# Kernel optimization log

Hardware: AMD Instinct MI355X
Metric: run time of the kernel (lower is better)

Reference implementation:

```python
import jax, jax.numpy as jnp
import numpy as np

B, J, D, H, W, AE, GH, NA, EH, L = 64, 20000, 32, 64, 4, 16, 24, 5000, 128, 32


def _ln(x, g=None, b=None, eps=1e-5):
    mu = x.mean(-1, keepdims=True)
    var = jnp.mean((x - mu) ** 2, axis=-1, keepdims=True)
    y = (x - mu) * jax.lax.rsqrt(var + eps)
    if g is not None:
        y = y * g + b
    return y


def setup_inputs():
    key = jax.random.key(0)
    ks = jax.random.split(key, 12)
    def rn(k, shape, s):
        return (jax.random.normal(k, shape) * s).astype(jnp.float32)
    return {
        "x": jax.random.normal(ks[0], (B, J), jnp.float32),
        "mask": jax.random.randint(ks[1], (B, J), 0, 2, jnp.int32),
        "atse_idx": jax.random.randint(ks[2], (J,), 0, NA, jnp.int32),
        "feature_embedding": jax.random.normal(ks[3], (J, D), jnp.float32),
        "atse_embedding": jax.random.normal(ks[4], (NA, AE), jnp.float32),
        "h_W1": rn(ks[5], (1 + D, H), 0.15), "h_b1": jnp.zeros((H,), jnp.float32),
        "h_ln1_g": jnp.ones((H,), jnp.float32), "h_ln1_b": jnp.zeros((H,), jnp.float32),
        "h_W2": rn(ks[6], (H, D), 0.12), "h_b2": jnp.zeros((D,), jnp.float32),
        "h_ln2_g": jnp.ones((D,), jnp.float32), "h_ln2_b": jnp.zeros((D,), jnp.float32),
        "g_W1": rn(ks[7], (D + AE, GH), 0.14), "g_b1": jnp.zeros((GH,), jnp.float32),
        "g_W2": rn(ks[8], (GH, W), 0.2), "g_b2": jnp.zeros((W,), jnp.float32),
        "c_W": rn(ks[9], (W * D, D), 0.09), "c_b": jnp.zeros((D,), jnp.float32),
        "c_ln_g": jnp.ones((D,), jnp.float32), "c_ln_b": jnp.zeros((D,), jnp.float32),
        "e_W1": rn(ks[10], (D, EH), 0.18), "e_b1": jnp.zeros((EH,), jnp.float32),
        "e_W2": rn(ks[11], (EH, 2 * L), 0.09), "e_b2": jnp.zeros((2 * L,), jnp.float32),
    }


def _forward(x, mask, atse_idx, feature_embedding, atse_embedding,
             h_W1, h_b1, h_ln1_g, h_ln1_b, h_W2, h_b2, h_ln2_g, h_ln2_b,
             g_W1, g_b1, g_W2, g_b2, c_W, c_b, c_ln_g, c_ln_b,
             e_W1, e_b1, e_W2, e_b2):
    TEMP = 1.0  # temperature_fixed=True -> scale = temperature_value
    Bv, Jv = x.shape
    Dv = feature_embedding.shape[1]
    # h-layer on all (b, j) pairs; LayerNorm/ReLU are per-row so this equals the
    # per-sample gather version on observed rows (unobserved rows get zero weight below).
    h_in = jnp.concatenate(
        [x[..., None], jnp.broadcast_to(feature_embedding[None], (Bv, Jv, Dv))], axis=-1)
    h = jax.nn.relu(_ln(h_in @ h_W1 + h_b1, h_ln1_g, h_ln1_b))
    h_out = jax.nn.relu(_ln(h @ h_W2 + h_b2, h_ln2_g, h_ln2_b))  # [B, J, D]
    # gate: [h_out | E_atse(j)] -> W head logits
    ae = atse_embedding[atse_idx]  # [J, AE]
    gate_in = jnp.concatenate(
        [h_out, jnp.broadcast_to(ae[None], (Bv, Jv, ae.shape[1]))], axis=-1)
    raw = jax.nn.relu(gate_in @ g_W1 + g_b1) @ g_W2 + g_b2  # [B, J, W]
    logits = jnp.clip(raw * TEMP, -10.0, 10.0)
    obs = mask.astype(bool)
    masked = jnp.where(obs[..., None], logits, -1e9)
    weights = jax.nn.softmax(masked, axis=1)  # softmax over observed junctions per head
    head_sums = jnp.einsum('bjw,bjd->bwd', weights, h_out)  # [B, W, D]
    Wn, Dn = head_sums.shape[1], head_sums.shape[2]
    combined = jax.nn.relu(_ln(head_sums.reshape(Bv, Wn * Dn) @ c_W + c_b, c_ln_g, c_ln_b))
    combined = jnp.where(obs.any(axis=1)[:, None], combined, 0.0)  # empty-mask rows -> zeros
    # encoder_mlp: scvi FCLayers, 2 layers, LayerNorm (no affine) + ReLU each
    e1 = jax.nn.relu(_ln(combined @ e_W1 + e_b1))
    mu_logvar = jax.nn.relu(_ln(e1 @ e_W2 + e_b2))
    mu, logvar = jnp.split(mu_logvar, 2, axis=-1)
    return mu, logvar


def reference(x, mask, atse_idx, feature_embedding, atse_embedding,
              h_W1, h_b1, h_ln1_g, h_ln1_b, h_W2, h_b2, h_ln2_g, h_ln2_b,
              g_W1, g_b1, g_W2, g_b2, c_W, c_b, c_ln_g, c_ln_b,
              e_W1, e_b1, e_W2, e_b2):
    return _forward(x, mask, atse_idx, feature_embedding, atse_embedding,
                    h_W1, h_b1, h_ln1_g, h_ln1_b, h_W2, h_b2, h_ln2_g, h_ln2_b,
                    g_W1, g_b1, g_W2, g_b2, c_W, c_b, c_ln_g, c_ln_b,
                    e_W1, e_b1, e_W2, e_b2)
```

## Files before the change

kernel.cpp:

```cpp
#include <hip/hip_runtime.h>
#include <hip/hip_bf16.h>
#include <math.h>

#define Bv 64
#define Jv 20000
#define NBT 8
#define NYB 125
#define ITERS 5

typedef __attribute__((ext_vector_type(8))) short short8;
typedef __attribute__((ext_vector_type(4))) float f32x4;
typedef __attribute__((ext_vector_type(2))) float f32x2;
typedef __attribute__((ext_vector_type(2))) unsigned int u32x2;

union U8 { short8 s; unsigned int u[4]; };

__device__ __forceinline__ unsigned short f2bf(float f) {
  unsigned int u = __float_as_uint(f);
  u += 0x7FFFu + ((u >> 16) & 1u);
  return (unsigned short)(u >> 16);
}
__device__ __forceinline__ unsigned int pkbf(float a, float b) {
  __hip_bfloat162 h = __float22bfloat162_rn(make_float2(a, b));
  union { __hip_bfloat162 h; unsigned int u; } c;
  c.h = h;
  return c.u;
}

__device__ __forceinline__ f32x2 pk_fma(f32x2 a, f32x2 b, f32x2 c) {
  return __builtin_elementwise_fma(a, b, c);
}
__device__ __forceinline__ f32x2 pk_max0(f32x2 a) {
  f32x2 z = {0.f, 0.f};
  return __builtin_elementwise_max(a, z);
}

template <int CTRL>
__device__ __forceinline__ float dppadd(float v) {
  int t = __builtin_amdgcn_update_dpp(0, __float_as_int(v), CTRL, 0xF, 0xF, true);
  return v + __int_as_float(t);
}
__device__ __forceinline__ float pl16sum(float v) {
  float a = v, b;
  asm("v_mov_b32 %1, %0\n\t"
      "v_permlane16_swap_b32 %0, %1"
      : "+v"(a), "=&v"(b));
  return a + b;
}
__device__ __forceinline__ float pl32sum(float v) {
  float a = v, b;
  asm("v_mov_b32 %1, %0\n\t"
      "v_permlane32_swap_b32 %0, %1"
      : "+v"(a), "=&v"(b));
  return a + b;
}

__global__ __launch_bounds__(256) void pe_fused(
    const float* __restrict__ x, const int* __restrict__ mask,
    const int* __restrict__ atse_idx, const float* __restrict__ fe,
    const float* __restrict__ ae,
    const float* __restrict__ hW1, const float* __restrict__ hb1,
    const float* __restrict__ hl1g, const float* __restrict__ hl1b,
    const float* __restrict__ hW2, const float* __restrict__ hb2,
    const float* __restrict__ hl2g, const float* __restrict__ hl2b,
    const float* __restrict__ gW1, const float* __restrict__ gb1,
    const float* __restrict__ gW2, const float* __restrict__ gb2,
    float* __restrict__ acc_g, float* __restrict__ se_g) {
  __shared__ __align__(16) float s_pg[32 * 68];
  __shared__ __align__(16) float s_gb[32 * 24 + 16];
  __shared__ __align__(16) float s_pair[256 * 4];
  __shared__ __align__(16) float s_w0[64], s_w0g[64], s_l1g[64], s_l1b[64];
  __shared__ __align__(16) float s_b2[32], s_l2g[32], s_l2b[32];
  __shared__ __align__(16) float s_gb1[24], s_gW2[96];
  __shared__ float s_gb2[4], s_scal[2];
  __shared__ __align__(16) float s_gW1aT[24 * 16];
  __shared__ unsigned char s_mk[256];
  __shared__ __align__(16) unsigned short s_gW1bf[32 * 24];
  __shared__ __align__(16) unsigned short s_ovl[256 * 36];

  int tid = threadIdx.x;
  int btile = blockIdx.x;
  int ytile = blockIdx.y;
  int lane = tid & 63, wv = tid >> 6;
  int li = lane & 15, quad = lane >> 4;
  unsigned short* s_h = s_ovl;

#define AEROW(j) ((float*)((char*)s_ovl + ((j) >> 3) * 4608 + 3968) + ((j) & 7) * 20)

  for (int i = tid; i < 768; i += 256) s_gW1bf[i] = f2bf(gW1[i]);
  for (int i = tid; i < 384; i += 256)
    s_gW1aT[i] = gW1[768 + (i & 15) * 24 + (i >> 4)];
  if (tid < 96) s_gW2[tid] = gW2[tid];
  if (tid < 64) { s_w0[tid] = hW1[tid]; s_l1g[tid] = hl1g[tid]; s_l1b[tid] = hl1b[tid]; }
  if (tid < 32) { s_b2[tid] = hb2[tid]; s_l2g[tid] = hl2g[tid]; s_l2b[tid] = hl2b[tid]; }
  if (tid < 24) s_gb1[tid] = gb1[tid];
  if (tid < 4) s_gb2[tid] = gb2[tid];
  if (tid >= 224 && tid < 240) s_gb[32 * 24 + (tid - 224)] = 0.f;

  short8 bW2[2][2];
#pragma unroll
  for (int kt = 0; kt < 2; ++kt)
#pragma unroll
    for (int nt = 0; nt < 2; ++nt) {
      U8 t;
#pragma unroll
      for (int p = 0; p < 4; ++p) {
        float lo = hW2[(kt * 32 + quad * 8 + 2 * p) * 32 + nt * 16 + li];
        float hi = hW2[(kt * 32 + quad * 8 + 2 * p + 1) * 32 + nt * 16 + li];
        t.u[p] = pkbf(lo, hi);
      }
      bW2[kt][nt] = t.s;
    }
  U8 bH;
#pragma unroll
  for (int p = 0; p < 4; ++p) {
    float lo = hW1[(1 + quad * 8 + 2 * p) * 64 + wv * 16 + li];
    float hi = hW1[(1 + quad * 8 + 2 * p + 1) * 64 + wv * 16 + li];
    bH.u[p] = pkbf(lo, hi);
  }
  float hb = hb1[wv * 16 + li];

  __syncthreads();
  if (tid < 64) s_w0g[tid] = s_w0[tid] * s_l1g[tid];
  if (tid == 64) {
    float sw = 0.f, qw = 0.f;
    for (int k = 0; k < 64; ++k) { float w = s_w0[k]; sw += w; qw = fmaf(w, w, qw); }
    s_scal[0] = sw; s_scal[1] = qw;
  }
  short8 aG0, aG1;
#pragma unroll
  for (int i = 0; i < 8; ++i) {
    int k = quad * 8 + i;
    aG0[i] = (short)s_gW1bf[k * 24 + li];
    aG1[i] = (li < 8) ? (short)s_gW1bf[k * 24 + 16 + li] : (short)0;
  }

  f32x4 racc[2][2];
#pragma unroll
  for (int a = 0; a < 2; ++a)
#pragma unroll
    for (int c = 0; c < 2; ++c) {
      racc[a][c][0] = 0.f; racc[a][c][1] = 0.f; racc[a][c][2] = 0.f; racc[a][c][3] = 0.f;
    }
  float seacc[2] = {0.f, 0.f};

  int jp8 = tid >> 3, b8 = tid & 7;

  for (int it = 0; it < ITERS; ++it) {
    int J0 = (ytile * ITERS + it) * 32;

    if (tid < 32) {
      int ai = atse_idx[J0 + tid];
      const float4* av4 = (const float4*)(ae + (size_t)ai * 16);
      float* ar = AEROW(tid);
#pragma unroll
      for (int q = 0; q < 4; ++q) *(float4*)(ar + q * 4) = av4[q];
    }
    size_t xoff = (size_t)(btile * 8 + b8) * Jv + J0 + jp8;
    float xv = x[xoff];
    int mk = mask[xoff];
    {
      f32x4 cP;
#pragma unroll
      for (int mt = 0; mt < 2; ++mt) {
        cP[0] = hb; cP[1] = hb; cP[2] = hb; cP[3] = hb;
        const float* fp = fe + (size_t)(J0 + mt * 16 + li) * 32 + quad * 8;
        float4 f0 = *(const float4*)fp;
        float4 f1 = *(const float4*)(fp + 4);
        U8 aF;
        aF.u[0] = pkbf(f0.x, f0.y); aF.u[1] = pkbf(f0.z, f0.w);
        aF.u[2] = pkbf(f1.x, f1.y); aF.u[3] = pkbf(f1.z, f1.w);
        cP = __builtin_amdgcn_mfma_f32_16x16x32_bf16(aF.s, bH.s, cP, 0, 0, 0);
#pragma unroll
        for (int r = 0; r < 4; ++r)
          s_pg[(mt * 16 + quad * 4 + r) * 68 + wv * 16 + li] = cP[r];
      }
    }
    __syncthreads();

    {
      int c0 = b8 * 3;
      const f32x2* ar2 = (const f32x2*)AEROW(jp8);
      f32x2 A[8];
#pragma unroll
      for (int a = 0; a < 8; ++a) A[a] = ar2[a];
#pragma unroll
      for (int c = 0; c < 3; ++c) {
        const f32x2* tr2 = (const f32x2*)(s_gW1aT + (c0 + c) * 16);
        f32x2 g2 = {s_gb1[c0 + c], 0.f};
#pragma unroll
        for (int a = 0; a < 8; ++a) g2 = pk_fma(A[a], tr2[a], g2);
        s_gb[jp8 * 24 + c0 + c] = g2.x + g2.y;
      }
    }
    {
      const f32x2* pp2 = (const f32x2*)(s_pg + jp8 * 68 + b8 * 8);
      const f32x2* ww2 = (const f32x2*)(s_w0 + b8 * 8);
      f32x2 p2[4] = {pp2[0], pp2[1], pp2[2], pp2[3]};
      f32x2 s2 = (p2[0] + p2[1]) + (p2[2] + p2[3]);
      f32x2 q2 = pk_fma(p2[0], p2[0],
                 pk_fma(p2[1], p2[1],
                 pk_fma(p2[2], p2[2], p2[3] * p2[3])));
      f32x2 d2 = pk_fma(p2[0], ww2[0],
                 pk_fma(p2[1], ww2[1],
                 pk_fma(p2[2], ww2[2], p2[3] * ww2[3])));
      float sp = s2.x + s2.y, qp = q2.x + q2.y, dwp = d2.x + d2.y;
      sp = dppadd<0xB1>(sp); sp = dppadd<0x4E>(sp); sp = dppadd<0x141>(sp);
      qp = dppadd<0xB1>(qp); qp = dppadd<0x4E>(qp); qp = dppadd<0x141>(qp);
      dwp = dppadd<0xB1>(dwp); dwp = dppadd<0x4E>(dwp); dwp = dppadd<0x141>(dwp);
      if (b8 == 0) *(float4*)(s_pg + jp8 * 68 + 64) = make_float4(sp, qp, dwp, 0.f);
    }
    {
      float4 exv = *(const float4*)(s_pg + jp8 * 68 + 64);
      float mu1 = fmaf(xv, s_scal[0], exv.x) * 0.015625f;
      float Et2 = fmaf(xv * xv, s_scal[1], fmaf(2.0f * xv, exv.z, exv.y)) * 0.015625f;
      float rs1 = rsqrtf(fmaxf(Et2 - mu1 * mu1, 0.f) + 1e-5f);
      *(float4*)(s_pair + tid * 4) = make_float4(xv * rs1, rs1, -mu1 * rs1, 0.f);
      s_mk[tid] = (unsigned char)mk;
    }

    {
      f32x4 cd[4][2];
      float b2a = s_b2[li], b2b = s_b2[16 + li];
#pragma unroll
      for (int t = 0; t < 4; ++t) {
        cd[t][0][0] = b2a; cd[t][0][1] = b2a; cd[t][0][2] = b2a; cd[t][0][3] = b2a;
        cd[t][1][0] = b2b; cd[t][1][1] = b2b; cd[t][1][2] = b2b; cd[t][1][3] = b2b;
      }
#pragma unroll
      for (int kt = 0; kt < 2; ++kt) {
        int base = kt * 32 + quad * 8;
        float4 wg0 = *(const float4*)(s_w0g + base);
        float4 wg1 = *(const float4*)(s_w0g + base + 4);
        float4 gg0 = *(const float4*)(s_l1g + base);
        float4 gg1 = *(const float4*)(s_l1g + base + 4);
        float4 bb0 = *(const float4*)(s_l1b + base);
        float4 bb1 = *(const float4*)(s_l1b + base + 4);
        f32x2 wg2[4] = {{wg0.x, wg0.y}, {wg0.z, wg0.w}, {wg1.x, wg1.y}, {wg1.z, wg1.w}};
        f32x2 gg2[4] = {{gg0.x, gg0.y}, {gg0.z, gg0.w}, {gg1.x, gg1.y}, {gg1.z, gg1.w}};
        f32x2 bb2[4] = {{bb0.x, bb0.y}, {bb0.z, bb0.w}, {bb1.x, bb1.y}, {bb1.z, bb1.w}};
#pragma unroll
        for (int t = 0; t < 4; ++t) {
          int mrow = wv * 64 + t * 16 + li;
          float4 pr = *(const float4*)(s_pair + mrow * 4);
          f32x2 prx = {pr.x, pr.x}, pry = {pr.y, pr.y}, prz = {pr.z, pr.z};
          const float* pgp = s_pg + (mrow >> 3) * 68 + base;
          float4 p0 = *(const float4*)pgp;
          float4 p1 = *(const float4*)(pgp + 4);
          f32x2 pv2[4] = {{p0.x, p0.y}, {p0.z, p0.w}, {p1.x, p1.y}, {p1.z, p1.w}};
          U8 a8;
#pragma unroll
          for (int i = 0; i < 4; ++i) {
            f32x2 av2 = pk_max0(pk_fma(pk_fma(pry, pv2[i], prz), gg2[i],
                                       pk_fma(prx, wg2[i], bb2[i])));
            a8.u[i] = pkbf(av2.x, av2.y);
          }
          cd[t][0] = __builtin_amdgcn_mfma_f32_16x16x32_bf16(a8.s, bW2[kt][0], cd[t][0], 0, 0, 0);
          cd[t][1] = __builtin_amdgcn_mfma_f32_16x16x32_bf16(a8.s, bW2[kt][1], cd[t][1], 0, 0, 0);
        }
      }
      float g0 = s_l2g[li], be0 = s_l2b[li];
      float g1v = s_l2g[16 + li], be1 = s_l2b[16 + li];
#pragma unroll
      for (int t = 0; t < 4; ++t) {
        float sum[4], sq[4];
#pragma unroll
        for (int r = 0; r < 4; ++r) {
          float a = cd[t][0][r], b = cd[t][1][r];
          sum[r] = a + b;
          sq[r] = fmaf(a, a, b * b);
        }
#pragma unroll
        for (int r = 0; r < 4; ++r) {
          sum[r] = dppadd<0xB1>(sum[r]); sum[r] = dppadd<0x4E>(sum[r]);
          sum[r] = dppadd<0x124>(sum[r]); sum[r] = dppadd<0x128>(sum[r]);
          sq[r] = dppadd<0xB1>(sq[r]); sq[r] = dppadd<0x4E>(sq[r]);
          sq[r] = dppadd<0x124>(sq[r]); sq[r] = dppadd<0x128>(sq[r]);
        }
#pragma unroll
        for (int r = 0; r < 4; ++r) {
          float mu = sum[r] * 0.03125f;
          float var = sq[r] * 0.03125f - mu * mu;
          float rs2 = rsqrtf(fmaxf(var, 0.f) + 1e-5f);
          int m = wv * 64 + t * 16 + quad * 4 + r;
          float h0 = fmaxf(fmaf((cd[t][0][r] - mu) * rs2, g0, be0), 0.f);
          float h1 = fmaxf(fmaf((cd[t][1][r] - mu) * rs2, g1v, be1), 0.f);
          s_h[m * 36 + li] = f2bf(h0);
          s_h[m * 36 + 16 + li] = f2bf(h1);
        }
      }
    }

    {
      float4 gw4[2][4];
#pragma unroll
      for (int mt = 0; mt < 2; ++mt)
#pragma unroll
        for (int r = 0; r < 4; ++r) {
          int c = mt * 16 + quad * 4 + r;
          gw4[mt][r] = (c < 24) ? ((const float4*)s_gW2)[c]
                                : make_float4(0.f, 0.f, 0.f, 0.f);
        }
#pragma unroll
      for (int nt = 0; nt < 4; ++nt) {
        int m = wv * 64 + nt * 16 + li;
        U8 bu;
        const u32x2* hp2 = (const u32x2*)(s_h + m * 36 + quad * 8);
        u32x2 h01 = hp2[0], h23 = hp2[1];
        bu.u[0] = h01[0]; bu.u[1] = h01[1]; bu.u[2] = h23[0]; bu.u[3] = h23[1];
        int j = m >> 3;
        f32x4 c0, c1;
#pragma unroll
        for (int r = 0; r < 4; ++r) {
          c0[r] = s_gb[j * 24 + quad * 4 + r];
          c1[r] = s_gb[j * 24 + 16 + quad * 4 + r];
        }
        c0 = __builtin_amdgcn_mfma_f32_16x16x32_bf16(aG0, bu.s, c0, 0, 0, 0);
        c1 = __builtin_amdgcn_mfma_f32_16x16x32_bf16(aG1, bu.s, c1, 0, 0, 0);
        f32x2 r01 = {s_gb2[0], s_gb2[1]};
        f32x2 r23 = {s_gb2[2], s_gb2[3]};
#pragma unroll
        for (int r = 0; r < 4; ++r) {
          float v0 = fmaxf(c0[r], 0.f);
          float v1 = fmaxf(c1[r], 0.f);
          f32x2 v0b = {v0, v0}, v1b = {v1, v1};
          float4 ga = gw4[0][r], gb = gw4[1][r];
          f32x2 ga01 = {ga.x, ga.y}, ga23 = {ga.z, ga.w};
          f32x2 gb01 = {gb.x, gb.y}, gb23 = {gb.z, gb.w};
          r01 = pk_fma(v0b, ga01, pk_fma(v1b, gb01, r01));
          r23 = pk_fma(v0b, ga23, pk_fma(v1b, gb23, r23));
        }
        float r0 = pl32sum(pl16sum(r01.x));
        float r1 = pl32sum(pl16sum(r01.y));
        float r2 = pl32sum(pl16sum(r23.x));
        float r3 = pl32sum(pl16sum(r23.y));
        r0 = fminf(fmaxf(r0, -10.f), 10.f);
        r1 = fminf(fmaxf(r1, -10.f), 10.f);
        r2 = fminf(fmaxf(r2, -10.f), 10.f);
        r3 = fminf(fmaxf(r3, -10.f), 10.f);
        bool act = (s_mk[m] != 0);
        float e0 = act ? __expf(r0 - 10.f) : 0.f;
        float e1 = act ? __expf(r1 - 10.f) : 0.f;
        float e2 = act ? __expf(r2 - 10.f) : 0.f;
        float e3 = act ? __expf(r3 - 10.f) : 0.f;
        if (quad == 0) *(float4*)(s_pair + m * 4) = make_float4(e0, e1, e2, e3);
      }
    }
    __syncthreads();

    {
      const float* s_e2 = s_pair;
#pragma unroll
      for (int bs = 0; bs < 2; ++bs) {
        int b = wv * 2 + bs;
        float ev[8];
        float sep = 0.f;
#pragma unroll
        for (int i = 0; i < 8; ++i) {
          float v = s_e2[((quad * 8 + i) * 8 + b) * 4 + (li & 3)];
          v = (li < 4) ? v : 0.f;
          ev[i] = v;
          sep += v;
        }
        seacc[bs] += sep;
        U8 a8;
        a8.u[0] = pkbf(ev[0], ev[1]); a8.u[1] = pkbf(ev[2], ev[3]);
        a8.u[2] = pkbf(ev[4], ev[5]); a8.u[3] = pkbf(ev[6], ev[7]);
#pragma unroll
        for (int half = 0; half < 2; ++half) {
          U8 bh;
#pragma unroll
          for (int p = 0; p < 4; ++p) {
            unsigned int lo = s_h[((quad * 8 + 2 * p) * 8 + b) * 36 + half * 16 + li];
            unsigned int hi = s_h[((quad * 8 + 2 * p + 1) * 8 + b) * 36 + half * 16 + li];
            bh.u[p] = lo | (hi << 16);
          }
          racc[bs][half] = __builtin_amdgcn_mfma_f32_16x16x32_bf16(a8.s, bh.s, racc[bs][half], 0, 0, 0);
        }
      }
    }
    __syncthreads();
  }

#pragma unroll
  for (int bs = 0; bs < 2; ++bs) {
    float se = seacc[bs];
    se = pl32sum(pl16sum(se));
    if (quad == 0) {
      int bg = btile * 8 + wv * 2 + bs;
      float* dst = acc_g + (size_t)bg * 128;
#pragma unroll
      for (int half = 0; half < 2; ++half)
#pragma unroll
        for (int r = 0; r < 4; ++r)
          atomicAdd(dst + r * 32 + half * 16 + li, racc[bs][half][r]);
      if (li < 4) atomicAdd(&se_g[bg * 4 + li], se);
    }
  }
#undef AEROW
}

__global__ __launch_bounds__(64) void pe_tail(
    const float* __restrict__ acc_g, const float* __restrict__ se_g,
    const float* __restrict__ cW, const float* __restrict__ cb,
    const float* __restrict__ clng, const float* __restrict__ clnb,
    const float* __restrict__ eW1, const float* __restrict__ eb1,
    const float* __restrict__ eW2, const float* __restrict__ eb2,
    float* __restrict__ out) {
  int b = blockIdx.x;
  int lane = threadIdx.x;
  __shared__ float s_hs[128], s_comb[32], s_e1[128];

  float se0 = se_g[b * 4 + 0];
  bool empty = !(se0 > 0.0f);
  float inv[4];
#pragma unroll
  for (int w = 0; w < 4; ++w) {
    float sw = se_g[b * 4 + w];
    inv[w] = empty ? 0.0f : 1.0f / sw;
  }
  s_hs[lane] = acc_g[b * 128 + lane] * inv[lane >> 5];
  s_hs[lane + 64] = acc_g[b * 128 + lane + 64] * inv[(lane + 64) >> 5];
  __syncthreads();

  if (lane < 32) {
    float cp = cb[lane];
#pragma unroll 8
    for (int i = 0; i < 128; ++i) cp = fmaf(s_hs[i], cW[i * 32 + lane], cp);
    float ssum = cp;
#pragma unroll
    for (int off = 16; off > 0; off >>= 1) ssum += __shfl_xor(ssum, off, 32);
    float mu = ssum * (1.0f / 32.0f);
    float dd = cp - mu;
    float sq = dd * dd;
#pragma unroll
    for (int off = 16; off > 0; off >>= 1) sq += __shfl_xor(sq, off, 32);
    float rs = rsqrtf(sq * (1.0f / 32.0f) + 1e-5f);
    float comb = fmaxf(fmaf(dd * rs, clng[lane], clnb[lane]), 0.0f);
    if (empty) comb = 0.0f;
    s_comb[lane] = comb;
  }
  __syncthreads();

  float v0 = eb1[lane], v1 = eb1[lane + 64];
#pragma unroll
  for (int i = 0; i < 32; ++i) {
    float c = s_comb[i];
    v0 = fmaf(c, eW1[i * 128 + lane], v0);
    v1 = fmaf(c, eW1[i * 128 + lane + 64], v1);
  }
  float ssum = v0 + v1;
#pragma unroll
  for (int off = 32; off > 0; off >>= 1) ssum += __shfl_xor(ssum, off, 64);
  float mu = ssum * (1.0f / 128.0f);
  float d0 = v0 - mu, d1 = v1 - mu;
  float sq = fmaf(d0, d0, d1 * d1);
#pragma unroll
  for (int off = 32; off > 0; off >>= 1) sq += __shfl_xor(sq, off, 64);
  float rs = rsqrtf(sq * (1.0f / 128.0f) + 1e-5f);
  s_e1[lane] = fmaxf(d0 * rs, 0.0f);
  s_e1[lane + 64] = fmaxf(d1 * rs, 0.0f);
  __syncthreads();

  float v = eb2[lane];
#pragma unroll 8
  for (int i = 0; i < 128; ++i) v = fmaf(s_e1[i], eW2[i * 64 + lane], v);
  ssum = v;
#pragma unroll
  for (int off = 32; off > 0; off >>= 1) ssum += __shfl_xor(ssum, off, 64);
  mu = ssum * (1.0f / 64.0f);
  float dv = v - mu;
  sq = dv * dv;
#pragma unroll
  for (int off = 32; off > 0; off >>= 1) sq += __shfl_xor(sq, off, 64);
  rs = rsqrtf(sq * (1.0f / 64.0f) + 1e-5f);
  float o = fmaxf(dv * rs, 0.0f);
  if (lane < 32)
    out[b * 32 + lane] = o;
  else
    out[Bv * 32 + b * 32 + (lane - 32)] = o;
}

extern "C" void kernel_launch(void* const* d_in, const int* in_sizes, int n_in,
                              void* d_out, int out_size, void* d_ws, size_t ws_size,
                              hipStream_t stream) {
  const float* x    = (const float*)d_in[0];
  const int* mask   = (const int*)d_in[1];
  const int* atse   = (const int*)d_in[2];
  const float* fe   = (const float*)d_in[3];
  const float* ae   = (const float*)d_in[4];
  const float* hW1  = (const float*)d_in[5];
  const float* hb1  = (const float*)d_in[6];
  const float* hl1g = (const float*)d_in[7];
  const float* hl1b = (const float*)d_in[8];
  const float* hW2  = (const float*)d_in[9];
  const float* hb2  = (const float*)d_in[10];
  const float* hl2g = (const float*)d_in[11];
  const float* hl2b = (const float*)d_in[12];
  const float* gW1  = (const float*)d_in[13];
  const float* gb1  = (const float*)d_in[14];
  const float* gW2  = (const float*)d_in[15];
  const float* gb2  = (const float*)d_in[16];
  const float* cW   = (const float*)d_in[17];
  const float* cb   = (const float*)d_in[18];
  const float* clng = (const float*)d_in[19];
  const float* clnb = (const float*)d_in[20];
  const float* eW1  = (const float*)d_in[21];
  const float* eb1  = (const float*)d_in[22];
  const float* eW2  = (const float*)d_in[23];
  const float* eb2  = (const float*)d_in[24];
  float* out = (float*)d_out;

  float* ws = (float*)d_ws;
  float* accg = ws;
  float* seg  = accg + Bv * 128;

  hipMemsetAsync(accg, 0, (Bv * 128 + Bv * 4) * sizeof(float), stream);

  pe_fused<<<dim3(NBT, NYB), dim3(256), 0, stream>>>(
      x, mask, atse, fe, ae, hW1, hb1, hl1g, hl1b, hW2, hb2, hl2g, hl2b,
      gW1, gb1, gW2, gb2, accg, seg);
  pe_tail<<<dim3(Bv), dim3(64), 0, stream>>>(
      accg, seg, cW, cb, clng, clnb, eW1, eb1, eW2, eb2, out);
}
```

Before: 212.0 us.

## Drop per-block junction loop; launch one block per 32-junction tile

Removes the 5-iteration loop over junction tiles inside each block and launches five times as many blocks along the junction axis, with each block handling a single 32-junction tile. Per-tile results are atomically added straight to the global accumulators instead of being held in registers across iterations. The change also loads the gate bias with float4 reads. The aim is more parallelism and fewer block-internal barriers, at the cost of five times the global atomics and repeating the per-block weight setup in every block.

```diff
diff --git a/kernel.cpp b/kernel.cpp
--- a/kernel.cpp
+++ b/kernel.cpp
@@ -5,8 +5,7 @@
 #define Bv 64
 #define Jv 20000
 #define NBT 8
-#define NYB 125
-#define ITERS 5
+#define NYB 625
 
 typedef __attribute__((ext_vector_type(8))) short short8;
 typedef __attribute__((ext_vector_type(4))) float f32x4;
@@ -87,6 +86,8 @@
 
 #define AEROW(j) ((float*)((char*)s_ovl + ((j) >> 3) * 4608 + 3968) + ((j) & 7) * 20)
 
+  int J0 = ytile * 32;
+
   for (int i = tid; i < 768; i += 256) s_gW1bf[i] = f2bf(gW1[i]);
   for (int i = tid; i < 384; i += 256)
     s_gW1aT[i] = gW1[768 + (i & 15) * 24 + (i >> 4)];
@@ -135,266 +136,244 @@
     aG1[i] = (li < 8) ? (short)s_gW1bf[k * 24 + 16 + li] : (short)0;
   }
 
-  f32x4 racc[2][2];
-#pragma unroll
-  for (int a = 0; a < 2; ++a)
-#pragma unroll
-    for (int c = 0; c < 2; ++c) {
-      racc[a][c][0] = 0.f; racc[a][c][1] = 0.f; racc[a][c][2] = 0.f; racc[a][c][3] = 0.f;
-    }
-  float seacc[2] = {0.f, 0.f};
-
   int jp8 = tid >> 3, b8 = tid & 7;
 
-  for (int it = 0; it < ITERS; ++it) {
-    int J0 = (ytile * ITERS + it) * 32;
-
-    if (tid < 32) {
-      int ai = atse_idx[J0 + tid];
-      const float4* av4 = (const float4*)(ae + (size_t)ai * 16);
-      float* ar = AEROW(tid);
-#pragma unroll
-      for (int q = 0; q < 4; ++q) *(float4*)(ar + q * 4) = av4[q];
-    }
-    size_t xoff = (size_t)(btile * 8 + b8) * Jv + J0 + jp8;
-    float xv = x[xoff];
-    int mk = mask[xoff];
-    {
-      f32x4 cP;
-#pragma unroll
-      for (int mt = 0; mt < 2; ++mt) {
-        cP[0] = hb; cP[1] = hb; cP[2] = hb; cP[3] = hb;
-        const float* fp = fe + (size_t)(J0 + mt * 16 + li) * 32 + quad * 8;
-        float4 f0 = *(const float4*)fp;
-        float4 f1 = *(const float4*)(fp + 4);
-        U8 aF;
-        aF.u[0] = pkbf(f0.x, f0.y); aF.u[1] = pkbf(f0.z, f0.w);
-        aF.u[2] = pkbf(f1.x, f1.y); aF.u[3] = pkbf(f1.z, f1.w);
-        cP = __builtin_amdgcn_mfma_f32_16x16x32_bf16(aF.s, bH.s, cP, 0, 0, 0);
-#pragma unroll
-        for (int r = 0; r < 4; ++r)
-          s_pg[(mt * 16 + quad * 4 + r) * 68 + wv * 16 + li] = cP[r];
-      }
-    }
-    __syncthreads();
-
-    {
-      int c0 = b8 * 3;
-      const f32x2* ar2 = (const f32x2*)AEROW(jp8);
-      f32x2 A[8];
-#pragma unroll
-      for (int a = 0; a < 8; ++a) A[a] = ar2[a];
-#pragma unroll
-      for (int c = 0; c < 3; ++c) {
-        const f32x2* tr2 = (const f32x2*)(s_gW1aT + (c0 + c) * 16);
-        f32x2 g2 = {s_gb1[c0 + c], 0.f};
-#pragma unroll
-        for (int a = 0; a < 8; ++a) g2 = pk_fma(A[a], tr2[a], g2);
-        s_gb[jp8 * 24 + c0 + c] = g2.x + g2.y;
-      }
-    }
-    {
-      const f32x2* pp2 = (const f32x2*)(s_pg + jp8 * 68 + b8 * 8);
-      const f32x2* ww2 = (const f32x2*)(s_w0 + b8 * 8);
-      f32x2 p2[4] = {pp2[0], pp2[1], pp2[2], pp2[3]};
-      f32x2 s2 = (p2[0] + p2[1]) + (p2[2] + p2[3]);
-      f32x2 q2 = pk_fma(p2[0], p2[0],
-                 pk_fma(p2[1], p2[1],
-                 pk_fma(p2[2], p2[2], p2[3] * p2[3])));
-      f32x2 d2 = pk_fma(p2[0], ww2[0],
-                 pk_fma(p2[1], ww2[1],
-                 pk_fma(p2[2], ww2[2], p2[3] * ww2[3])));
-      float sp = s2.x + s2.y, qp = q2.x + q2.y, dwp = d2.x + d2.y;
-      sp = dppadd<0xB1>(sp); sp = dppadd<0x4E>(sp); sp = dppadd<0x141>(sp);
-      qp = dppadd<0xB1>(qp); qp = dppadd<0x4E>(qp); qp = dppadd<0x141>(qp);
-      dwp = dppadd<0xB1>(dwp); dwp = dppadd<0x4E>(dwp); dwp = dppadd<0x141>(dwp);
-      if (b8 == 0) *(float4*)(s_pg + jp8 * 68 + 64) = make_float4(sp, qp, dwp, 0.f);
-    }
-    {
-      float4 exv = *(const float4*)(s_pg + jp8 * 68 + 64);
-      float mu1 = fmaf(xv, s_scal[0], exv.x) * 0.015625f;
-      float Et2 = fmaf(xv * xv, s_scal[1], fmaf(2.0f * xv, exv.z, exv.y)) * 0.015625f;
-      float rs1 = rsqrtf(fmaxf(Et2 - mu1 * mu1, 0.f) + 1e-5f);
-      *(float4*)(s_pair + tid * 4) = make_float4(xv * rs1, rs1, -mu1 * rs1, 0.f);
-      s_mk[tid] = (unsigned char)mk;
-    }
-
-    {
-      f32x4 cd[4][2];
-      float b2a = s_b2[li], b2b = s_b2[16 + li];
+  if (tid < 32) {
+    int ai = atse_idx[J0 + tid];
+    const float4* av4 = (const float4*)(ae + (size_t)ai * 16);
+    float* ar = AEROW(tid);
+#pragma unroll
+    for (int q = 0; q < 4; ++q) *(float4*)(ar + q * 4) = av4[q];
+  }
+  size_t xoff = (size_t)(btile * 8 + b8) * Jv + J0 + jp8;
+  float xv = x[xoff];
+  int mk = mask[xoff];
+  {
+    f32x4 cP;
+#pragma unroll
+    for (int mt = 0; mt < 2; ++mt) {
+      cP[0] = hb; cP[1] = hb; cP[2] = hb; cP[3] = hb;
+      const float* fp = fe + (size_t)(J0 + mt * 16 + li) * 32 + quad * 8;
+      float4 f0 = *(const float4*)fp;
+      float4 f1 = *(const float4*)(fp + 4);
+      U8 aF;
+      aF.u[0] = pkbf(f0.x, f0.y); aF.u[1] = pkbf(f0.z, f0.w);
+      aF.u[2] = pkbf(f1.x, f1.y); aF.u[3] = pkbf(f1.z, f1.w);
+      cP = __builtin_amdgcn_mfma_f32_16x16x32_bf16(aF.s, bH.s, cP, 0, 0, 0);
+#pragma unroll
+      for (int r = 0; r < 4; ++r)
+        s_pg[(mt * 16 + quad * 4 + r) * 68 + wv * 16 + li] = cP[r];
+    }
+  }
+  __syncthreads();
+
+  {
+    int c0 = b8 * 3;
+    const f32x2* ar2 = (const f32x2*)AEROW(jp8);
+    f32x2 A[8];
+#pragma unroll
+    for (int a = 0; a < 8; ++a) A[a] = ar2[a];
+#pragma unroll
+    for (int c = 0; c < 3; ++c) {
+      const f32x2* tr2 = (const f32x2*)(s_gW1aT + (c0 + c) * 16);
+      f32x2 g2 = {s_gb1[c0 + c], 0.f};
+#pragma unroll
+      for (int a = 0; a < 8; ++a) g2 = pk_fma(A[a], tr2[a], g2);
+      s_gb[jp8 * 24 + c0 + c] = g2.x + g2.y;
+    }
+  }
+  {
+    const f32x2* pp2 = (const f32x2*)(s_pg + jp8 * 68 + b8 * 8);
+    const f32x2* ww2 = (const f32x2*)(s_w0 + b8 * 8);
+    f32x2 p2[4] = {pp2[0], pp2[1], pp2[2], pp2[3]};
+    f32x2 s2 = (p2[0] + p2[1]) + (p2[2] + p2[3]);
+    f32x2 q2 = pk_fma(p2[0], p2[0],
+               pk_fma(p2[1], p2[1],
+               pk_fma(p2[2], p2[2], p2[3] * p2[3])));
+    f32x2 d2 = pk_fma(p2[0], ww2[0],
+               pk_fma(p2[1], ww2[1],
+               pk_fma(p2[2], ww2[2], p2[3] * ww2[3])));
+    float sp = s2.x + s2.y, qp = q2.x + q2.y, dwp = d2.x + d2.y;
+    sp = dppadd<0xB1>(sp); sp = dppadd<0x4E>(sp); sp = dppadd<0x141>(sp);
+    qp = dppadd<0xB1>(qp); qp = dppadd<0x4E>(qp); qp = dppadd<0x141>(qp);
+    dwp = dppadd<0xB1>(dwp); dwp = dppadd<0x4E>(dwp); dwp = dppadd<0x141>(dwp);
+    if (b8 == 0) *(float4*)(s_pg + jp8 * 68 + 64) = make_float4(sp, qp, dwp, 0.f);
+  }
+  {
+    float4 exv = *(const float4*)(s_pg + jp8 * 68 + 64);
+    float mu1 = fmaf(xv, s_scal[0], exv.x) * 0.015625f;
+    float Et2 = fmaf(xv * xv, s_scal[1], fmaf(2.0f * xv, exv.z, exv.y)) * 0.015625f;
+    float rs1 = rsqrtf(fmaxf(Et2 - mu1 * mu1, 0.f) + 1e-5f);
+    *(float4*)(s_pair + tid * 4) = make_float4(xv * rs1, rs1, -mu1 * rs1, 0.f);
+    s_mk[tid] = (unsigned char)mk;
+  }
+
+  {
+    f32x4 cd[4][2];
+    float b2a = s_b2[li], b2b = s_b2[16 + li];
+#pragma unroll
+    for (int t = 0; t < 4; ++t) {
+      cd[t][0][0] = b2a; cd[t][0][1] = b2a; cd[t][0][2] = b2a; cd[t][0][3] = b2a;
+      cd[t][1][0] = b2b; cd[t][1][1] = b2b; cd[t][1][2] = b2b; cd[t][1][3] = b2b;
+    }
+#pragma unroll
+    for (int kt = 0; kt < 2; ++kt) {
+      int base = kt * 32 + quad * 8;
+      float4 wg0 = *(const float4*)(s_w0g + base);
+      float4 wg1 = *(const float4*)(s_w0g + base + 4);
+      float4 gg0 = *(const float4*)(s_l1g + base);
+      float4 gg1 = *(const float4*)(s_l1g + base + 4);
+      float4 bb0 = *(const float4*)(s_l1b + base);
+      float4 bb1 = *(const float4*)(s_l1b + base + 4);
+      f32x2 wg2[4] = {{wg0.x, wg0.y}, {wg0.z, wg0.w}, {wg1.x, wg1.y}, {wg1.z, wg1.w}};
+      f32x2 gg2[4] = {{gg0.x, gg0.y}, {gg0.z, gg0.w}, {gg1.x, gg1.y}, {gg1.z, gg1.w}};
+      f32x2 bb2[4] = {{bb0.x, bb0.y}, {bb0.z, bb0.w}, {bb1.x, bb1.y}, {bb1.z, bb1.w}};
 #pragma unroll
       for (int t = 0; t < 4; ++t) {
-        cd[t][0][0] = b2a; cd[t][0][1] = b2a; cd[t][0][2] = b2a; cd[t][0][3] = b2a;
-        cd[t][1][0] = b2b; cd[t][1][1] = b2b; cd[t][1][2] = b2b; cd[t][1][3] = b2b;
-      }
-#pragma unroll
-      for (int kt = 0; kt < 2; ++kt) {
-        int base = kt * 32 + quad * 8;
-        float4 wg0 = *(const float4*)(s_w0g + base);
-        float4 wg1 = *(const float4*)(s_w0g + base + 4);
-        float4 gg0 = *(const float4*)(s_l1g + base);
-        float4 gg1 = *(const float4*)(s_l1g + base + 4);
-        float4 bb0 = *(const float4*)(s_l1b + base);
-        float4 bb1 = *(const float4*)(s_l1b + base + 4);
-        f32x2 wg2[4] = {{wg0.x, wg0.y}, {wg0.z, wg0.w}, {wg1.x, wg1.y}, {wg1.z, wg1.w}};
-        f32x2 gg2[4] = {{gg0.x, gg0.y}, {gg0.z, gg0.w}, {gg1.x, gg1.y}, {gg1.z, gg1.w}};
-        f32x2 bb2[4] = {{bb0.x, bb0.y}, {bb0.z, bb0.w}, {bb1.x, bb1.y}, {bb1.z, bb1.w}};
-#pragma unroll
-        for (int t = 0; t < 4; ++t) {
-          int mrow = wv * 64 + t * 16 + li;
-          float4 pr = *(const float4*)(s_pair + mrow * 4);
-          f32x2 prx = {pr.x, pr.x}, pry = {pr.y, pr.y}, prz = {pr.z, pr.z};
-          const float* pgp = s_pg + (mrow >> 3) * 68 + base;
-          float4 p0 = *(const float4*)pgp;
-          float4 p1 = *(const float4*)(pgp + 4);
-          f32x2 pv2[4] = {{p0.x, p0.y}, {p0.z, p0.w}, {p1.x, p1.y}, {p1.z, p1.w}};
-          U8 a8;
-#pragma unroll
-          for (int i = 0; i < 4; ++i) {
-            f32x2 av2 = pk_max0(pk_fma(pk_fma(pry, pv2[i], prz), gg2[i],
-                                       pk_fma(prx, wg2[i], bb2[i])));
-            a8.u[i] = pkbf(av2.x, av2.y);
-          }
-          cd[t][0] = __builtin_amdgcn_mfma_f32_16x16x32_bf16(a8.s, bW2[kt][0], cd[t][0], 0, 0, 0);
-          cd[t][1] = __builtin_amdgcn_mfma_f32_16x16x32_bf16(a8.s, bW2[kt][1], cd[t][1], 0, 0, 0);
+        int mrow = wv * 64 + t * 16 + li;
+        float4 pr = *(const float4*)(s_pair + mrow * 4);
+        f32x2 prx = {pr.x, pr.x}, pry = {pr.y, pr.y}, prz = {pr.z, pr.z};
+        const float* pgp = s_pg + (mrow >> 3) * 68 + base;
+        float4 p0 = *(const float4*)pgp;
+        float4 p1 = *(const float4*)(pgp + 4);
+        f32x2 pv2[4] = {{p0.x, p0.y}, {p0.z, p0.w}, {p1.x, p1.y}, {p1.z, p1.w}};
+        U8 a8;
+#pragma unroll
+        for (int i = 0; i < 4; ++i) {
+          f32x2 av2 = pk_max0(pk_fma(pk_fma(pry, pv2[i], prz), gg2[i],
+                                     pk_fma(prx, wg2[i], bb2[i])));
+          a8.u[i] = pkbf(av2.x, av2.y);
         }
-      }
-      float g0 = s_l2g[li], be0 = s_l2b[li];
-      float g1v = s_l2g[16 + li], be1 = s_l2b[16 + li];
-#pragma unroll
-      for (int t = 0; t < 4; ++t) {
-        float sum[4], sq[4];
-#pragma unroll
-        for (int r = 0; r < 4; ++r) {
-          float a = cd[t][0][r], b = cd[t][1][r];
-          sum[r] = a + b;
-          sq[r] = fmaf(a, a, b * b);
+        cd[t][0] = __builtin_amdgcn_mfma_f32_16x16x32_bf16(a8.s, bW2[kt][0], cd[t][0], 0, 0, 0);
+        cd[t][1] = __builtin_amdgcn_mfma_f32_16x16x32_bf16(a8.s, bW2[kt][1], cd[t][1], 0, 0, 0);
+      }
+    }
+    float g0 = s_l2g[li], be0 = s_l2b[li];
+    float g1v = s_l2g[16 + li], be1 = s_l2b[16 + li];
+#pragma unroll
+    for (int t = 0; t < 4; ++t) {
+      float sum[4], sq[4];
+#pragma unroll
+      for (int r = 0; r < 4; ++r) {
+        float a = cd[t][0][r], b = cd[t][1][r];
+        sum[r] = a + b;
+        sq[r] = fmaf(a, a, b * b);
+      }
+#pragma unroll
+      for (int r = 0; r < 4; ++r) {
+        sum[r] = dppadd<0xB1>(sum[r]); sum[r] = dppadd<0x4E>(sum[r]);
+        sum[r] = dppadd<0x124>(sum[r]); sum[r] = dppadd<0x128>(sum[r]);
+        sq[r] = dppadd<0xB1>(sq[r]); sq[r] = dppadd<0x4E>(sq[r]);
+        sq[r] = dppadd<0x124>(sq[r]); sq[r] = dppadd<0x128>(sq[r]);
+      }
+#pragma unroll
+      for (int r = 0; r < 4; ++r) {
+        float mu = sum[r] * 0.03125f;
+        float var = sq[r] * 0.03125f - mu * mu;
+        float rs2 = rsqrtf(fmaxf(var, 0.f) + 1e-5f);
+        int m = wv * 64 + t * 16 + quad * 4 + r;
+        float h0 = fmaxf(fmaf((cd[t][0][r] - mu) * rs2, g0, be0), 0.f);
+        float h1 = fmaxf(fmaf((cd[t][1][r] - mu) * rs2, g1v, be1), 0.f);
+        s_h[m * 36 + li] = f2bf(h0);
+        s_h[m * 36 + 16 + li] = f2bf(h1);
+      }
+    }
+  }
+
+  {
+    float4 gw4[2][4];
+#pragma unroll
+    for (int mt = 0; mt < 2; ++mt)
+#pragma unroll
+      for (int r = 0; r < 4; ++r) {
+        int c = mt * 16 + quad * 4 + r;
+        gw4[mt][r] = (c < 24) ? ((const float4*)s_gW2)[c]
+                              : make_float4(0.f, 0.f, 0.f, 0.f);
+      }
+#pragma unroll
+    for (int nt = 0; nt < 4; ++nt) {
+      int m = wv * 64 + nt * 16 + li;
+      U8 bu;
+      const u32x2* hp2 = (const u32x2*)(s_h + m * 36 + quad * 8);
+      u32x2 h01 = hp2[0], h23 = hp2[1];
+      bu.u[0] = h01[0]; bu.u[1] = h01[1]; bu.u[2] = h23[0]; bu.u[3] = h23[1];
+      int j = m >> 3;
+      float4 cc0 = *(const float4*)(s_gb + j * 24 + quad * 4);
+      float4 cc1 = *(const float4*)(s_gb + j * 24 + 16 + quad * 4);
+      f32x4 c0, c1;
+      c0[0] = cc0.x; c0[1] = cc0.y; c0[2] = cc0.z; c0[3] = cc0.w;
+      c1[0] = cc1.x; c1[1] = cc1.y; c1[2] = cc1.z; c1[3] = cc1.w;
+      c0 = __builtin_amdgcn_mfma_f32_16x16x32_bf16(aG0, bu.s, c0, 0, 0, 0);
+      c1 = __builtin_amdgcn_mfma_f32_16x16x32_bf16(aG1, bu.s, c1, 0, 0, 0);
+      f32x2 r01 = {s_gb2[0], s_gb2[1]};
+      f32x2 r23 = {s_gb2[2], s_gb2[3]};
+#pragma unroll
+      for (int r = 0; r < 4; ++r) {
+        float v0 = fmaxf(c0[r], 0.f);
+        float v1 = fmaxf(c1[r], 0.f);
+        f32x2 v0b = {v0, v0}, v1b = {v1, v1};
+        float4 ga = gw4[0][r], gb = gw4[1][r];
+        f32x2 ga01 = {ga.x, ga.y}, ga23 = {ga.z, ga.w};
+        f32x2 gb01 = {gb.x, gb.y}, gb23 = {gb.z, gb.w};
+        r01 = pk_fma(v0b, ga01, pk_fma(v1b, gb01, r01));
+        r23 = pk_fma(v0b, ga23, pk_fma(v1b, gb23, r23));
+      }
+      float r0 = pl32sum(pl16sum(r01.x));
+      float r1 = pl32sum(pl16sum(r01.y));
+      float r2 = pl32sum(pl16sum(r23.x));
+      float r3 = pl32sum(pl16sum(r23.y));
+      r0 = fminf(fmaxf(r0, -10.f), 10.f);
+      r1 = fminf(fmaxf(r1, -10.f), 10.f);
+      r2 = fminf(fmaxf(r2, -10.f), 10.f);
+      r3 = fminf(fmaxf(r3, -10.f), 10.f);
+      bool act = (s_mk[m] != 0);
+      float e0 = act ? __expf(r0 - 10.f) : 0.f;
+      float e1 = act ? __expf(r1 - 10.f) : 0.f;
+      float e2 = act ? __expf(r2 - 10.f) : 0.f;
+      float e3 = act ? __expf(r3 - 10.f) : 0.f;
+      if (quad == 0) *(float4*)(s_pair + m * 4) = make_float4(e0, e1, e2, e3);
+    }
+  }
+  __syncthreads();
+
+  {
+    const float* s_e2 = s_pair;
+#pragma unroll
+    for (int bs = 0; bs < 2; ++bs) {
+      int b = wv * 2 + bs;
+      float ev[8];
+      float sep = 0.f;
+#pragma unroll
+      for (int i = 0; i < 8; ++i) {
+        float v = s_e2[((quad * 8 + i) * 8 + b) * 4 + (li & 3)];
+        v = (li < 4) ? v : 0.f;
+        ev[i] = v;
+        sep += v;
+      }
+      sep = pl32sum(pl16sum(sep));
+      U8 a8;
+      a8.u[0] = pkbf(ev[0], ev[1]); a8.u[1] = pkbf(ev[2], ev[3]);
+      a8.u[2] = pkbf(ev[4], ev[5]); a8.u[3] = pkbf(ev[6], ev[7]);
+#pragma unroll
+      for (int half = 0; half < 2; ++half) {
+        U8 bh;
+#pragma unroll
+        for (int p = 0; p < 4; ++p) {
+          unsigned int lo = s_h[((quad * 8 + 2 * p) * 8 + b) * 36 + half * 16 + li];
+          unsigned int hi = s_h[((quad * 8 + 2 * p + 1) * 8 + b) * 36 + half * 16 + li];
+          bh.u[p] = lo | (hi << 16);
         }
-#pragma unroll
-        for (int r = 0; r < 4; ++r) {
-          sum[r] = dppadd<0xB1>(sum[r]); sum[r] = dppadd<0x4E>(sum[r]);
-          sum[r] = dppadd<0x124>(sum[r]); sum[r] = dppadd<0x128>(sum[r]);
-          sq[r] = dppadd<0xB1>(sq[r]); sq[r] = dppadd<0x4E>(sq[r]);
-          sq[r] = dppadd<0x124>(sq[r]); sq[r] = dppadd<0x128>(sq[r]);
+        f32x4 c = {0.f, 0.f, 0.f, 0.f};
+        c = __builtin_amdgcn_mfma_f32_16x16x32_bf16(a8.s, bh.s, c, 0, 0, 0);
+        if (quad == 0) {
+          float* dst = acc_g + (size_t)(btile * 8 + b) * 128;
+#pragma unroll
+          for (int r = 0; r < 4; ++r)
+            atomicAdd(dst + r * 32 + half * 16 + li, c[r]);
         }
-#pragma unroll
-        for (int r = 0; r < 4; ++r) {
-          float mu = sum[r] * 0.03125f;
-          float var = sq[r] * 0.03125f - mu * mu;
-          float rs2 = rsqrtf(fmaxf(var, 0.f) + 1e-5f);
-          int m = wv * 64 + t * 16 + quad * 4 + r;
-          float h0 = fmaxf(fmaf((cd[t][0][r] - mu) * rs2, g0, be0), 0.f);
-          float h1 = fmaxf(fmaf((cd[t][1][r] - mu) * rs2, g1v, be1), 0.f);
-          s_h[m * 36 + li] = f2bf(h0);
-          s_h[m * 36 + 16 + li] = f2bf(h1);
-        }
-      }
-    }
-
-    {
-      float4 gw4[2][4];
-#pragma unroll
-      for (int mt = 0; mt < 2; ++mt)
-#pragma unroll
-        for (int r = 0; r < 4; ++r) {
-          int c = mt * 16 + quad * 4 + r;
-          gw4[mt][r] = (c < 24) ? ((const float4*)s_gW2)[c]
-                                : make_float4(0.f, 0.f, 0.f, 0.f);
-        }
-#pragma unroll
-      for (int nt = 0; nt < 4; ++nt) {
-        int m = wv * 64 + nt * 16 + li;
-        U8 bu;
-        const u32x2* hp2 = (const u32x2*)(s_h + m * 36 + quad * 8);
-        u32x2 h01 = hp2[0], h23 = hp2[1];
-        bu.u[0] = h01[0]; bu.u[1] = h01[1]; bu.u[2] = h23[0]; bu.u[3] = h23[1];
-        int j = m >> 3;
-        f32x4 c0, c1;
-#pragma unroll
-        for (int r = 0; r < 4; ++r) {
-          c0[r] = s_gb[j * 24 + quad * 4 + r];
-          c1[r] = s_gb[j * 24 + 16 + quad * 4 + r];
-        }
-        c0 = __builtin_amdgcn_mfma_f32_16x16x32_bf16(aG0, bu.s, c0, 0, 0, 0);
-        c1 = __builtin_amdgcn_mfma_f32_16x16x32_bf16(aG1, bu.s, c1, 0, 0, 0);
-        f32x2 r01 = {s_gb2[0], s_gb2[1]};
-        f32x2 r23 = {s_gb2[2], s_gb2[3]};
-#pragma unroll
-        for (int r = 0; r < 4; ++r) {
-          float v0 = fmaxf(c0[r], 0.f);
-          float v1 = fmaxf(c1[r], 0.f);
-          f32x2 v0b = {v0, v0}, v1b = {v1, v1};
-          float4 ga = gw4[0][r], gb = gw4[1][r];
-          f32x2 ga01 = {ga.x, ga.y}, ga23 = {ga.z, ga.w};
-          f32x2 gb01 = {gb.x, gb.y}, gb23 = {gb.z, gb.w};
-          r01 = pk_fma(v0b, ga01, pk_fma(v1b, gb01, r01));
-          r23 = pk_fma(v0b, ga23, pk_fma(v1b, gb23, r23));
-        }
-        float r0 = pl32sum(pl16sum(r01.x));
-        float r1 = pl32sum(pl16sum(r01.y));
-        float r2 = pl32sum(pl16sum(r23.x));
-        float r3 = pl32sum(pl16sum(r23.y));
-        r0 = fminf(fmaxf(r0, -10.f), 10.f);
-        r1 = fminf(fmaxf(r1, -10.f), 10.f);
-        r2 = fminf(fmaxf(r2, -10.f), 10.f);
-        r3 = fminf(fmaxf(r3, -10.f), 10.f);
-        bool act = (s_mk[m] != 0);
-        float e0 = act ? __expf(r0 - 10.f) : 0.f;
-        float e1 = act ? __expf(r1 - 10.f) : 0.f;
-        float e2 = act ? __expf(r2 - 10.f) : 0.f;
-        float e3 = act ? __expf(r3 - 10.f) : 0.f;
-        if (quad == 0) *(float4*)(s_pair + m * 4) = make_float4(e0, e1, e2, e3);
-      }
-    }
-    __syncthreads();
-
-    {
-      const float* s_e2 = s_pair;
-#pragma unroll
-      for (int bs = 0; bs < 2; ++bs) {
-        int b = wv * 2 + bs;
-        float ev[8];
-        float sep = 0.f;
-#pragma unroll
-        for (int i = 0; i < 8; ++i) {
-          float v = s_e2[((quad * 8 + i) * 8 + b) * 4 + (li & 3)];
-          v = (li < 4) ? v : 0.f;
-          ev[i] = v;
-          sep += v;
-        }
-        seacc[bs] += sep;
-        U8 a8;
-        a8.u[0] = pkbf(ev[0], ev[1]); a8.u[1] = pkbf(ev[2], ev[3]);
-        a8.u[2] = pkbf(ev[4], ev[5]); a8.u[3] = pkbf(ev[6], ev[7]);
-#pragma unroll
-        for (int half = 0; half < 2; ++half) {
-          U8 bh;
-#pragma unroll
-          for (int p = 0; p < 4; ++p) {
-            unsigned int lo = s_h[((quad * 8 + 2 * p) * 8 + b) * 36 + half * 16 + li];
-            unsigned int hi = s_h[((quad * 8 + 2 * p + 1) * 8 + b) * 36 + half * 16 + li];
-            bh.u[p] = lo | (hi << 16);
-          }
-          racc[bs][half] = __builtin_amdgcn_mfma_f32_16x16x32_bf16(a8.s, bh.s, racc[bs][half], 0, 0, 0);
-        }
-      }
-    }
-    __syncthreads();
-  }
-
-#pragma unroll
-  for (int bs = 0; bs < 2; ++bs) {
-    float se = seacc[bs];
-    se = pl32sum(pl16sum(se));
-    if (quad == 0) {
-      int bg = btile * 8 + wv * 2 + bs;
-      float* dst = acc_g + (size_t)bg * 128;
-#pragma unroll
-      for (int half = 0; half < 2; ++half)
-#pragma unroll
-        for (int r = 0; r < 4; ++r)
-          atomicAdd(dst + r * 32 + half * 16 + li, racc[bs][half][r]);
-      if (li < 4) atomicAdd(&se_g[bg * 4 + li], se);
+      }
+      if (quad == 0 && li < 4)
+        atomicAdd(&se_g[(btile * 8 + b) * 4 + li], sep);
     }
   }
 #undef AEROW
```

New measurement: 221.4 us. +4.5%, slower.

## Software-pipeline next-tile global loads behind the softmax-weighted reduction

Applied to the files above, without the earlier changes.

Restructures the per-iteration loop so the next tile's atse, feature-embedding, x and mask loads are issued before the weighted-sum MFMA stage and consumed after it. This hides global latency and removes one barrier per iteration. It also moves the atse-embedding rows out of the overlapped scratch into a dedicated shared array, aliases the bf16 gW1 copy onto s_pair, vectorises the s_gb bias loads, and adds a two-blocks-per-CU launch bound. The trade-off is more live registers for the prefetched values, which the occupancy hint may constrain into spills.

```diff
diff --git a/kernel.cpp b/kernel.cpp
--- a/kernel.cpp
+++ b/kernel.cpp
@@ -55,7 +55,7 @@
   return a + b;
 }
 
-__global__ __launch_bounds__(256) void pe_fused(
+__global__ __launch_bounds__(256, 2) void pe_fused(
     const float* __restrict__ x, const int* __restrict__ mask,
     const int* __restrict__ atse_idx, const float* __restrict__ fe,
     const float* __restrict__ ae,
@@ -69,13 +69,13 @@
   __shared__ __align__(16) float s_pg[32 * 68];
   __shared__ __align__(16) float s_gb[32 * 24 + 16];
   __shared__ __align__(16) float s_pair[256 * 4];
+  __shared__ __align__(16) float s_ae[32 * 20];
   __shared__ __align__(16) float s_w0[64], s_w0g[64], s_l1g[64], s_l1b[64];
   __shared__ __align__(16) float s_b2[32], s_l2g[32], s_l2b[32];
   __shared__ __align__(16) float s_gb1[24], s_gW2[96];
   __shared__ float s_gb2[4], s_scal[2];
   __shared__ __align__(16) float s_gW1aT[24 * 16];
   __shared__ unsigned char s_mk[256];
-  __shared__ __align__(16) unsigned short s_gW1bf[32 * 24];
   __shared__ __align__(16) unsigned short s_ovl[256 * 36];
 
   int tid = threadIdx.x;
@@ -84,8 +84,7 @@
   int lane = tid & 63, wv = tid >> 6;
   int li = lane & 15, quad = lane >> 4;
   unsigned short* s_h = s_ovl;
-
-#define AEROW(j) ((float*)((char*)s_ovl + ((j) >> 3) * 4608 + 3968) + ((j) & 7) * 20)
+  unsigned short* s_gW1bf = (unsigned short*)s_pair;
 
   for (int i = tid; i < 768; i += 256) s_gW1bf[i] = f2bf(gW1[i]);
   for (int i = tid; i < 384; i += 256)
@@ -145,42 +144,41 @@
   float seacc[2] = {0.f, 0.f};
 
   int jp8 = tid >> 3, b8 = tid & 7;
+  int J0 = ytile * ITERS * 32;
+  float xv; int mk;
+
+  {
+    if (tid < 128) {
+      int jj = tid >> 2, q = tid & 3;
+      int ai = atse_idx[J0 + jj];
+      float4 av = *(const float4*)(ae + (size_t)ai * 16 + q * 4);
+      *(float4*)(s_ae + jj * 20 + q * 4) = av;
+    }
+    size_t xo = (size_t)(btile * 8 + b8) * Jv + J0 + jp8;
+    xv = x[xo];
+    mk = mask[xo];
+    f32x4 cP;
+#pragma unroll
+    for (int mt = 0; mt < 2; ++mt) {
+      cP[0] = hb; cP[1] = hb; cP[2] = hb; cP[3] = hb;
+      const float* fp = fe + (size_t)(J0 + mt * 16 + li) * 32 + quad * 8;
+      float4 f0 = *(const float4*)fp;
+      float4 f1 = *(const float4*)(fp + 4);
+      U8 aF;
+      aF.u[0] = pkbf(f0.x, f0.y); aF.u[1] = pkbf(f0.z, f0.w);
+      aF.u[2] = pkbf(f1.x, f1.y); aF.u[3] = pkbf(f1.z, f1.w);
+      cP = __builtin_amdgcn_mfma_f32_16x16x32_bf16(aF.s, bH.s, cP, 0, 0, 0);
+#pragma unroll
+      for (int r = 0; r < 4; ++r)
+        s_pg[(mt * 16 + quad * 4 + r) * 68 + wv * 16 + li] = cP[r];
+    }
+  }
+  __syncthreads();
 
   for (int it = 0; it < ITERS; ++it) {
-    int J0 = (ytile * ITERS + it) * 32;
-
-    if (tid < 32) {
-      int ai = atse_idx[J0 + tid];
-      const float4* av4 = (const float4*)(ae + (size_t)ai * 16);
-      float* ar = AEROW(tid);
-#pragma unroll
-      for (int q = 0; q < 4; ++q) *(float4*)(ar + q * 4) = av4[q];
-    }
-    size_t xoff = (size_t)(btile * 8 + b8) * Jv + J0 + jp8;
-    float xv = x[xoff];
-    int mk = mask[xoff];
-    {
-      f32x4 cP;
-#pragma unroll
-      for (int mt = 0; mt < 2; ++mt) {
-        cP[0] = hb; cP[1] = hb; cP[2] = hb; cP[3] = hb;
-        const float* fp = fe + (size_t)(J0 + mt * 16 + li) * 32 + quad * 8;
-        float4 f0 = *(const float4*)fp;
-        float4 f1 = *(const float4*)(fp + 4);
-        U8 aF;
-        aF.u[0] = pkbf(f0.x, f0.y); aF.u[1] = pkbf(f0.z, f0.w);
-        aF.u[2] = pkbf(f1.x, f1.y); aF.u[3] = pkbf(f1.z, f1.w);
-        cP = __builtin_amdgcn_mfma_f32_16x16x32_bf16(aF.s, bH.s, cP, 0, 0, 0);
-#pragma unroll
-        for (int r = 0; r < 4; ++r)
-          s_pg[(mt * 16 + quad * 4 + r) * 68 + wv * 16 + li] = cP[r];
-      }
-    }
-    __syncthreads();
-
     {
       int c0 = b8 * 3;
-      const f32x2* ar2 = (const f32x2*)AEROW(jp8);
+      const f32x2* ar2 = (const f32x2*)(s_ae + jp8 * 20);
       f32x2 A[8];
 #pragma unroll
       for (int a = 0; a < 8; ++a) A[a] = ar2[a];
@@ -309,12 +307,11 @@
         u32x2 h01 = hp2[0], h23 = hp2[1];
         bu.u[0] = h01[0]; bu.u[1] = h01[1]; bu.u[2] = h23[0]; bu.u[3] = h23[1];
         int j = m >> 3;
+        float4 cc0 = *(const float4*)(s_gb + j * 24 + quad * 4);
+        float4 cc1 = *(const float4*)(s_gb + j * 24 + 16 + quad * 4);
         f32x4 c0, c1;
-#pragma unroll
-        for (int r = 0; r < 4; ++r) {
-          c0[r] = s_gb[j * 24 + quad * 4 + r];
-          c1[r] = s_gb[j * 24 + 16 + quad * 4 + r];
-        }
+        c0[0] = cc0.x; c0[1] = cc0.y; c0[2] = cc0.z; c0[3] = cc0.w;
+        c1[0] = cc1.x; c1[1] = cc1.y; c1[2] = cc1.z; c1[3] = cc1.w;
         c0 = __builtin_amdgcn_mfma_f32_16x16x32_bf16(aG0, bu.s, c0, 0, 0, 0);
         c1 = __builtin_amdgcn_mfma_f32_16x16x32_bf16(aG1, bu.s, c1, 0, 0, 0);
         f32x2 r01 = {s_gb2[0], s_gb2[1]};
@@ -348,6 +345,24 @@
     }
     __syncthreads();
 
+    bool has_next = (it + 1 < ITERS);
+    int J0n = J0 + 32;
+    float4 nf0, nf1, nf2, nf3, nav;
+    float nxv = 0.f; int nmk = 0;
+    if (has_next) {
+      if (tid < 128) {
+        int jj = tid >> 2, q = tid & 3;
+        int ai = atse_idx[J0n + jj];
+        nav = *(const float4*)(ae + (size_t)ai * 16 + q * 4);
+      }
+      const float* fp0 = fe + (size_t)(J0n + li) * 32 + quad * 8;
+      const float* fp1 = fe + (size_t)(J0n + 16 + li) * 32 + quad * 8;
+      nf0 = *(const float4*)fp0; nf1 = *(const float4*)(fp0 + 4);
+      nf2 = *(const float4*)fp1; nf3 = *(const float4*)(fp1 + 4);
+      size_t xo = (size_t)(btile * 8 + b8) * Jv + J0n + jp8;
+      nxv = x[xo];
+      nmk = mask[xo];
+    }
     {
       const float* s_e2 = s_pair;
 #pragma unroll
@@ -379,7 +394,32 @@
         }
       }
     }
-    __syncthreads();
+    if (has_next) {
+      if (tid < 128) {
+        int jj = tid >> 2, q = tid & 3;
+        *(float4*)(s_ae + jj * 20 + q * 4) = nav;
+      }
+      f32x4 cP;
+#pragma unroll
+      for (int mt = 0; mt < 2; ++mt) {
+        cP[0] = hb; cP[1] = hb; cP[2] = hb; cP[3] = hb;
+        U8 aF;
+        if (mt == 0) {
+          aF.u[0] = pkbf(nf0.x, nf0.y); aF.u[1] = pkbf(nf0.z, nf0.w);
+          aF.u[2] = pkbf(nf1.x, nf1.y); aF.u[3] = pkbf(nf1.z, nf1.w);
+        } else {
+          aF.u[0] = pkbf(nf2.x, nf2.y); aF.u[1] = pkbf(nf2.z, nf2.w);
+          aF.u[2] = pkbf(nf3.x, nf3.y); aF.u[3] = pkbf(nf3.z, nf3.w);
+        }
+        cP = __builtin_amdgcn_mfma_f32_16x16x32_bf16(aF.s, bH.s, cP, 0, 0, 0);
+#pragma unroll
+        for (int r = 0; r < 4; ++r)
+          s_pg[(mt * 16 + quad * 4 + r) * 68 + wv * 16 + li] = cP[r];
+      }
+      xv = nxv; mk = nmk;
+      J0 = J0n;
+      __syncthreads();
+    }
   }
 
 #pragma unroll
@@ -397,7 +437,6 @@
       if (li < 4) atomicAdd(&se_g[bg * 4 + li], se);
     }
   }
-#undef AEROW
 }
 
 __global__ __launch_bounds__(64) void pe_tail(
```

Measured after the change: 209.7 us. Within noise of the previous version (-1.1%).
